# Performance work log

Hardware: AMD Instinct MI355X
Metric: run time of the kernel (lower is better)

The kernel has to match this reference:

```python
import jax, jax.numpy as jnp
import numpy as np

B, C, H, L = 8, 1, 512, 4096


def setup_inputs() -> dict:
    key = jax.random.key(0)
    k1, k2, k3, k4, k5 = jax.random.split(key, 5)
    u = jax.random.normal(k1, (B, H, L), dtype=jnp.float32)
    # SSM kernel k (C, H, L): stand-in for HippoSSKernel output, scaled so the
    # length-L convolution has O(1) variance.
    k = jax.random.normal(k2, (C, H, L), dtype=jnp.float32) * (1.0 / np.sqrt(L))
    D = jax.random.normal(k3, (C, H), dtype=jnp.float32)
    # output_linear: pointwise linear (C*H) -> H
    W = jax.random.normal(k4, (H, C * H), dtype=jnp.float32) * (1.0 / np.sqrt(C * H))
    b = jax.random.normal(k5, (H,), dtype=jnp.float32) * 0.01
    return {"u": u, "k": k, "D": D, "W": W, "b": b}


def reference(u, k, D, W, b):
    # u: (B, H, L), k: (C, H, L), D: (C, H), W: (H, C*H), b: (H,)
    Lq = u.shape[-1]
    n = 2 * Lq  # zero-padded FFT length for linear (non-circular) convolution
    k_f = jnp.fft.rfft(k, n=n)                       # (C, H, n//2+1) complex
    u_f = jnp.fft.rfft(u, n=n)                       # (B, H, n//2+1) complex
    y_f = jnp.einsum('bhl,chl->bchl', u_f, k_f)      # freq-domain multiply
    y = jnp.fft.irfft(y_f, n=n)[..., :Lq]            # (B, C, H, L)
    y = y + jnp.einsum('bhl,ch->bchl', u, D)         # skip term
    Bq, Cq, Hq, _ = y.shape
    y = y.reshape(Bq, Cq * Hq, Lq)                   # (B, C*H, L)
    y = jax.nn.gelu(y, approximate=False)            # torch GELU (erf)
    y = jnp.einsum('bcl,dc->bdl', y, W) + b[None, :, None]  # pointwise linear
    return y
```

## Files before the change

### kernel.cpp

```cpp
#include <hip/hip_runtime.h>
#include <hip/hip_bf16.h>
#include <math.h>

#define L_DIM 4096
#define H_DIM 512
#define B_DIM 8
#define SEG 2048

typedef __attribute__((ext_vector_type(8))) short short8;
typedef __attribute__((ext_vector_type(4))) float floatx4;

__device__ __forceinline__ unsigned f2bf(float f) {
    unsigned x = __float_as_uint(f);
    return (x + 0x7fffu + ((x >> 16) & 1u)) >> 16;
}

__global__ __launch_bounds__(256, 3) void conv_gelu_mfma(
    const float* __restrict__ u,
    const float* __restrict__ kk,
    const float* __restrict__ Dp,
    unsigned short* __restrict__ g)
{
    __shared__ __align__(16) unsigned short kA[4144];
    __shared__ __align__(16) unsigned short kB[4144];
    __shared__ __align__(16) unsigned short us[8][2104];

    const int h   = blockIdx.x;
    const int Lb  = blockIdx.y << 10;
    const int tid = threadIdx.x;
    const int lane = tid & 63;
    const int w   = tid >> 6;
    const int i   = lane & 15;
    const int q   = lane >> 4;
    const int b   = i & 7;
    const int s   = i >> 3;

    const float* kh = kk + (size_t)h * L_DIM;

    for (int p = tid; p < 4144; p += 256) {
        int t1 = L_DIM + 15 - p;
        int t2 = L_DIM + 14 - p;
        float v1 = (t1 >= 0 && t1 < L_DIM) ? kh[t1] : 0.0f;
        float v2 = (t2 >= 0 && t2 < L_DIM) ? kh[t2] : 0.0f;
        kA[p] = (unsigned short)f2bf(v1);
        kB[p] = (unsigned short)f2bf(v2);
    }

    floatx4 acc[8];
    #pragma unroll
    for (int t = 0; t < 8; t++) acc[t] = (floatx4){0.f, 0.f, 0.f, 0.f};

    const char* kbase = (const char*)((i & 1) ? kA : kB);
    const int aconst = 2 * (L_DIM + ((i & 1) ? 15 : 14) - i + 8 * q);
    const int basew = Lb + 32 * w;

    for (int seg = 0; seg < 2; seg++) {
        const int ms = seg * SEG;
        const int mstart = (seg == 0) ? -32 : SEG;
        const int segmax = ms + SEG - 32;
        if (seg == 1) {
            if (Lb + 992 < SEG) break;
            __syncthreads();
        }
        for (int e = tid * 4; e < 2096; e += 1024) {
            int m = ms - 32 + e;
            #pragma unroll
            for (int bb = 0; bb < 8; bb++) {
                float4 v = make_float4(0.f, 0.f, 0.f, 0.f);
                if (m >= 0 && m < L_DIM)
                    v = *(const float4*)(u + ((size_t)bb * H_DIM + h) * L_DIM + m);
                unsigned lo = f2bf(v.x) | (f2bf(v.y) << 16);
                unsigned hi = f2bf(v.z) | (f2bf(v.w) << 16);
                *(uint2*)&us[bb][e] = make_uint2(lo, hi);
            }
        }
        __syncthreads();

        const char* bbase = (const char*)&us[b][0] + 2 * (32 - ms + 16 * s + 8 * q);
        const char* ab = kbase + aconst;

        for (int c = 0; c < 4; c++) {
            const int c32 = 32 * c;
            const int rel = basew - c32;
            const int j_hi = (rel - mstart) >> 7;
            int j_lo = (rel - segmax + 127) >> 7;
            if (j_lo < -7) j_lo = -7;
            if (j_hi < j_lo) continue;
            const int n = j_hi - j_lo + 1;

            union AFrag { int x[4]; short8 v; };
            AFrag Wd[8];
            #pragma unroll
            for (int d = 1; d < 8; d++) {
                const int dd = c32 + (j_hi + d) * 128;
                if (dd >= 0) {
                    const int* ap = (const int*)(ab - 2 * dd);
                    Wd[d].x[0] = ap[0]; Wd[d].x[1] = ap[1];
                    Wd[d].x[2] = ap[2]; Wd[d].x[3] = ap[3];
                } else {
                    Wd[d].x[0] = 0; Wd[d].x[1] = 0; Wd[d].x[2] = 0; Wd[d].x[3] = 0;
                }
            }

            const char* aab = ab - 2 * c32 - 256 * j_hi;
            const char* bb0 = bbase + 2 * (rel - 128 * j_hi);

            for (int jb = 0; jb < n; jb += 8) {
                #pragma unroll
                for (int k = 0; k < 8; k++) {
                    const int jj = jb + k;
                    if (jj < n) {
                        const int dd0 = c32 + (j_hi - jj) * 128;
                        AFrag nf;
                        if (dd0 >= 0) {
                            const int* ap = (const int*)(aab + 256 * jj);
                            nf.x[0] = ap[0]; nf.x[1] = ap[1];
                            nf.x[2] = ap[2]; nf.x[3] = ap[3];
                        } else {
                            nf.x[0] = 0; nf.x[1] = 0; nf.x[2] = 0; nf.x[3] = 0;
                        }
                        Wd[(8 - k) & 7] = nf;
                        short8 bf = *(const short8*)(bb0 + 256 * jj);
                        #pragma unroll
                        for (int t = 0; t < 8; t++)
                            acc[t] = __builtin_amdgcn_mfma_f32_16x16x32_bf16(
                                Wd[(t - k) & 7].v, bf, acc[t], 0, 0, 0);
                    }
                }
            }
        }
    }

    const float Dh = Dp[h];
    #pragma unroll
    for (int t = 0; t < 8; t++) {
        const int l0 = Lb + 32 * w + 128 * t;
        const int lb2 = l0 + 16 * s + 4 * q;
        const size_t off = ((size_t)b * H_DIM + h) * L_DIM + lb2;
        float4 uv = *(const float4*)(u + off);
        float y0 = acc[t][0] + uv.x * Dh;
        float y1 = acc[t][1] + uv.y * Dh;
        float y2 = acc[t][2] + uv.z * Dh;
        float y3 = acc[t][3] + uv.w * Dh;
        const float c = 0.70710678118654752f;
        float g0 = 0.5f * y0 * (1.0f + erff(y0 * c));
        float g1 = 0.5f * y1 * (1.0f + erff(y1 * c));
        float g2 = 0.5f * y2 * (1.0f + erff(y2 * c));
        float g3 = 0.5f * y3 * (1.0f + erff(y3 * c));
        unsigned lo = f2bf(g0) | (f2bf(g1) << 16);
        unsigned hi = f2bf(g2) | (f2bf(g3) << 16);
        *(uint2*)(g + off) = make_uint2(lo, hi);
    }
}

__global__ __launch_bounds__(256, 2) void pointwise_mfma(
    const unsigned short* __restrict__ g,
    const float* __restrict__ W,
    const float* __restrict__ bias,
    float* __restrict__ out)
{
    __shared__ __align__(16) unsigned gs2[128 * 36];
    __shared__ __align__(16) unsigned short ws[256 * 72];

    const int tid = threadIdx.x;
    const int l0 = blockIdx.x * 128;
    const int d0 = blockIdx.y * 256;
    const int bz = blockIdx.z;
    const int w  = tid >> 6;
    const int lane = tid & 63;
    const int n  = lane & 15;
    const int q  = lane >> 4;

    const int p   = tid & 31;
    const int oct = tid >> 5;

    const int quarter = tid & 3;
    const int rb      = tid >> 2;

    floatx4 acc[8][4];
    #pragma unroll
    for (int mt = 0; mt < 8; mt++)
        #pragma unroll
        for (int nt = 0; nt < 4; nt++) acc[mt][nt] = (floatx4){0.f, 0.f, 0.f, 0.f};

    for (int c0 = 0; c0 < H_DIM; c0 += 64) {
        {
            const unsigned short* gp = g + ((size_t)bz * H_DIM + c0 + 2 * p) * L_DIM + l0 + 16 * oct;
            uint4 va0 = *(const uint4*)gp;
            uint4 va1 = *(const uint4*)(gp + 8);
            uint4 vb0 = *(const uint4*)(gp + L_DIM);
            uint4 vb1 = *(const uint4*)(gp + L_DIM + 8);
            #pragma unroll
            for (int half = 0; half < 2; half++) {
                const unsigned* ua = (const unsigned*)(half ? &va1 : &va0);
                const unsigned* ub = (const unsigned*)(half ? &vb1 : &vb0);
                #pragma unroll
                for (int e = 0; e < 4; e++) {
                    unsigned w0 = (ua[e] & 0xFFFFu) | (ub[e] << 16);
                    unsigned w1 = (ua[e] >> 16) | (ub[e] & 0xFFFF0000u);
                    const int lrow = 16 * oct + 8 * half + 2 * e;
                    gs2[lrow * 36 + p] = w0;
                    gs2[(lrow + 1) * 36 + p] = w1;
                }
            }
        }
        {
            #pragma unroll
            for (int gg = 0; gg < 4; gg++) {
                const int row = rb + 64 * gg;
                const float* wp = W + (size_t)(d0 + row) * H_DIM + c0 + 16 * quarter;
                float4 f0 = ((const float4*)wp)[0];
                float4 f1 = ((const float4*)wp)[1];
                float4 f2 = ((const float4*)wp)[2];
                float4 f3 = ((const float4*)wp)[3];
                unsigned o0 = f2bf(f0.x) | (f2bf(f0.y) << 16);
                unsigned o1 = f2bf(f0.z) | (f2bf(f0.w) << 16);
                unsigned o2 = f2bf(f1.x) | (f2bf(f1.y) << 16);
                unsigned o3 = f2bf(f1.z) | (f2bf(f1.w) << 16);
                unsigned o4 = f2bf(f2.x) | (f2bf(f2.y) << 16);
                unsigned o5 = f2bf(f2.z) | (f2bf(f2.w) << 16);
                unsigned o6 = f2bf(f3.x) | (f2bf(f3.y) << 16);
                unsigned o7 = f2bf(f3.z) | (f2bf(f3.w) << 16);
                *(uint4*)&ws[row * 72 + 16 * quarter]     = make_uint4(o0, o1, o2, o3);
                *(uint4*)&ws[row * 72 + 16 * quarter + 8] = make_uint4(o4, o5, o6, o7);
            }
        }
        __syncthreads();

        #pragma unroll
        for (int ks = 0; ks < 2; ks++) {
            short8 bfr[4];
            #pragma unroll
            for (int nt = 0; nt < 4; nt++)
                bfr[nt] = *(const short8*)&ws[(64 * w + 16 * nt + n) * 72 + 32 * ks + 8 * q];
            #pragma unroll
            for (int mt = 0; mt < 8; mt++) {
                union { uint4 u4; short8 v; } af;
                af.u4 = *(const uint4*)&gs2[(16 * mt + n) * 36 + 16 * ks + 4 * q];
                #pragma unroll
                for (int nt = 0; nt < 4; nt++)
                    acc[mt][nt] = __builtin_amdgcn_mfma_f32_16x16x32_bf16(af.v, bfr[nt], acc[mt][nt], 0, 0, 0);
            }
        }
        __syncthreads();
    }

    #pragma unroll
    for (int nt = 0; nt < 4; nt++) {
        const int d = d0 + 64 * w + 16 * nt + n;
        const float bb = bias[d];
        float* obase = out + ((size_t)bz * H_DIM + d) * L_DIM + l0 + 4 * q;
        #pragma unroll
        for (int mt = 0; mt < 8; mt++) {
            float4 r = make_float4(acc[mt][nt][0] + bb, acc[mt][nt][1] + bb,
                                   acc[mt][nt][2] + bb, acc[mt][nt][3] + bb);
            *(float4*)(obase + 16 * mt) = r;
        }
    }
}

extern "C" void kernel_launch(void* const* d_in, const int* in_sizes, int n_in,
                              void* d_out, int out_size, void* d_ws, size_t ws_size,
                              hipStream_t stream) {
    const float* u    = (const float*)d_in[0];
    const float* k    = (const float*)d_in[1];
    const float* D    = (const float*)d_in[2];
    const float* W    = (const float*)d_in[3];
    const float* bias = (const float*)d_in[4];
    float* out = (float*)d_out;
    unsigned short* g = (unsigned short*)d_ws;

    conv_gelu_mfma<<<dim3(H_DIM, L_DIM / 1024), 256, 0, stream>>>(u, k, D, g);
    pointwise_mfma<<<dim3(L_DIM / 128, H_DIM / 256, B_DIM), 256, 0, stream>>>(g, W, bias, out);
}
```

Baseline: 279.6 us.

## Widen conv blocks to 512 threads, pre-convert W to bf16, split pointwise warps

The conv+GELU kernel now uses 512-thread blocks that each cover 2048 output positions. The u staging is split into four 1024-wide segments to keep shared memory small, and the Toeplitz loop strides are adjusted to match. The conv kernel also converts W to bf16 once into spare workspace, so the pointwise GEMM can load bf16 weights directly instead of converting fp32 in every block. The pointwise kernel moves to 512 threads with a 2x4 warp split over the tile and wider LDS padding, which lowers per-thread accumulator pressure. The risk is lower MFMA reuse per wave and more conv blocks hitting redundant segment passes.

```diff
diff --git a/kernel.cpp b/kernel.cpp
--- a/kernel.cpp
+++ b/kernel.cpp
@@ -5,7 +5,7 @@
 #define L_DIM 4096
 #define H_DIM 512
 #define B_DIM 8
-#define SEG 2048
+#define SEG 1024
 
 typedef __attribute__((ext_vector_type(8))) short short8;
 typedef __attribute__((ext_vector_type(4))) float floatx4;
@@ -15,18 +15,20 @@
     return (x + 0x7fffu + ((x >> 16) & 1u)) >> 16;
 }
 
-__global__ __launch_bounds__(256, 3) void conv_gelu_mfma(
+__global__ __launch_bounds__(512, 8) void conv_gelu_mfma(
     const float* __restrict__ u,
     const float* __restrict__ kk,
     const float* __restrict__ Dp,
-    unsigned short* __restrict__ g)
+    unsigned short* __restrict__ g,
+    const float* __restrict__ W,
+    unsigned short* __restrict__ Wb)
 {
     __shared__ __align__(16) unsigned short kA[4144];
     __shared__ __align__(16) unsigned short kB[4144];
-    __shared__ __align__(16) unsigned short us[8][2104];
+    __shared__ __align__(16) unsigned short us[8][1080];
 
     const int h   = blockIdx.x;
-    const int Lb  = blockIdx.y << 10;
+    const int Lb  = blockIdx.y << 11;
     const int tid = threadIdx.x;
     const int lane = tid & 63;
     const int w   = tid >> 6;
@@ -35,9 +37,15 @@
     const int b   = i & 7;
     const int s   = i >> 3;
 
+    if (Wb != nullptr && blockIdx.y == 0) {
+        const float* wsrc = W + (size_t)h * H_DIM;
+        unsigned short* wdst = Wb + (size_t)h * H_DIM;
+        wdst[tid] = (unsigned short)f2bf(wsrc[tid]);
+    }
+
     const float* kh = kk + (size_t)h * L_DIM;
 
-    for (int p = tid; p < 4144; p += 256) {
+    for (int p = tid; p < 4144; p += 512) {
         int t1 = L_DIM + 15 - p;
         int t2 = L_DIM + 14 - p;
         float v1 = (t1 >= 0 && t1 < L_DIM) ? kh[t1] : 0.0f;
@@ -54,15 +62,17 @@
     const int aconst = 2 * (L_DIM + ((i & 1) ? 15 : 14) - i + 8 * q);
     const int basew = Lb + 32 * w;
 
-    for (int seg = 0; seg < 2; seg++) {
+    union AFrag { int x[4]; short8 v; };
+
+    for (int seg = 0; seg < 4; seg++) {
         const int ms = seg * SEG;
-        const int mstart = (seg == 0) ? -32 : SEG;
+        const int mstart = (seg == 0) ? -32 : ms;
         const int segmax = ms + SEG - 32;
-        if (seg == 1) {
-            if (Lb + 992 < SEG) break;
+        if (seg >= 1) {
+            if (Lb + 2016 < ms) break;
             __syncthreads();
         }
-        for (int e = tid * 4; e < 2096; e += 1024) {
+        for (int e = tid * 4; e < SEG + 48; e += 2048) {
             int m = ms - 32 + e;
             #pragma unroll
             for (int bb = 0; bb < 8; bb++) {
@@ -79,20 +89,19 @@
         const char* bbase = (const char*)&us[b][0] + 2 * (32 - ms + 16 * s + 8 * q);
         const char* ab = kbase + aconst;
 
-        for (int c = 0; c < 4; c++) {
+        for (int c = 0; c < 8; c++) {
             const int c32 = 32 * c;
             const int rel = basew - c32;
-            const int j_hi = (rel - mstart) >> 7;
-            int j_lo = (rel - segmax + 127) >> 7;
+            const int j_hi = (rel - mstart) >> 8;
+            int j_lo = (rel - segmax + 255) >> 8;
             if (j_lo < -7) j_lo = -7;
             if (j_hi < j_lo) continue;
             const int n = j_hi - j_lo + 1;
 
-            union AFrag { int x[4]; short8 v; };
             AFrag Wd[8];
             #pragma unroll
             for (int d = 1; d < 8; d++) {
-                const int dd = c32 + (j_hi + d) * 128;
+                const int dd = c32 + (j_hi + d) * 256;
                 if (dd >= 0) {
                     const int* ap = (const int*)(ab - 2 * dd);
                     Wd[d].x[0] = ap[0]; Wd[d].x[1] = ap[1];
@@ -102,25 +111,25 @@
                 }
             }
 
-            const char* aab = ab - 2 * c32 - 256 * j_hi;
-            const char* bb0 = bbase + 2 * (rel - 128 * j_hi);
+            const char* aab = ab - 2 * c32 - 512 * j_hi;
+            const char* bb0 = bbase + 2 * (rel - 256 * j_hi);
 
             for (int jb = 0; jb < n; jb += 8) {
                 #pragma unroll
                 for (int k = 0; k < 8; k++) {
                     const int jj = jb + k;
                     if (jj < n) {
-                        const int dd0 = c32 + (j_hi - jj) * 128;
+                        const int dd0 = c32 + (j_hi - jj) * 256;
                         AFrag nf;
                         if (dd0 >= 0) {
-                            const int* ap = (const int*)(aab + 256 * jj);
+                            const int* ap = (const int*)(aab + 512 * jj);
                             nf.x[0] = ap[0]; nf.x[1] = ap[1];
                             nf.x[2] = ap[2]; nf.x[3] = ap[3];
                         } else {
                             nf.x[0] = 0; nf.x[1] = 0; nf.x[2] = 0; nf.x[3] = 0;
                         }
                         Wd[(8 - k) & 7] = nf;
-                        short8 bf = *(const short8*)(bb0 + 256 * jj);
+                        short8 bf = *(const short8*)(bb0 + 512 * jj);
                         #pragma unroll
                         for (int t = 0; t < 8; t++)
                             acc[t] = __builtin_amdgcn_mfma_f32_16x16x32_bf16(
@@ -134,7 +143,7 @@
     const float Dh = Dp[h];
     #pragma unroll
     for (int t = 0; t < 8; t++) {
-        const int l0 = Lb + 32 * w + 128 * t;
+        const int l0 = Lb + 32 * w + 256 * t;
         const int lb2 = l0 + 16 * s + 4 * q;
         const size_t off = ((size_t)b * H_DIM + h) * L_DIM + lb2;
         float4 uv = *(const float4*)(u + off);
@@ -153,14 +162,16 @@
     }
 }
 
-__global__ __launch_bounds__(256, 2) void pointwise_mfma(
+template <bool PREW>
+__global__ __launch_bounds__(512, 4) void pointwise_mfma(
     const unsigned short* __restrict__ g,
+    const unsigned short* __restrict__ Wb,
     const float* __restrict__ W,
     const float* __restrict__ bias,
     float* __restrict__ out)
 {
-    __shared__ __align__(16) unsigned gs2[128 * 36];
-    __shared__ __align__(16) unsigned short ws[256 * 72];
+    __shared__ __align__(16) unsigned gs2[128 * 40];
+    __shared__ __align__(16) unsigned short ws[256 * 76];
 
     const int tid = threadIdx.x;
     const int l0 = blockIdx.x * 128;
@@ -170,44 +181,53 @@
     const int lane = tid & 63;
     const int n  = lane & 15;
     const int q  = lane >> 4;
+    const int wh = w & 1;
+    const int wd = w >> 1;
 
     const int p   = tid & 31;
-    const int oct = tid >> 5;
+    const int oct = (tid >> 5) & 7;
+    const int hi  = tid >> 8;
 
     const int quarter = tid & 3;
-    const int rb      = tid >> 2;
-
-    floatx4 acc[8][4];
+    const int rb      = (tid >> 2) & 63;
+
+    floatx4 acc[4][4];
     #pragma unroll
-    for (int mt = 0; mt < 8; mt++)
+    for (int mt = 0; mt < 4; mt++)
         #pragma unroll
         for (int nt = 0; nt < 4; nt++) acc[mt][nt] = (floatx4){0.f, 0.f, 0.f, 0.f};
 
     for (int c0 = 0; c0 < H_DIM; c0 += 64) {
         {
-            const unsigned short* gp = g + ((size_t)bz * H_DIM + c0 + 2 * p) * L_DIM + l0 + 16 * oct;
-            uint4 va0 = *(const uint4*)gp;
-            uint4 va1 = *(const uint4*)(gp + 8);
-            uint4 vb0 = *(const uint4*)(gp + L_DIM);
-            uint4 vb1 = *(const uint4*)(gp + L_DIM + 8);
-            #pragma unroll
-            for (int half = 0; half < 2; half++) {
-                const unsigned* ua = (const unsigned*)(half ? &va1 : &va0);
-                const unsigned* ub = (const unsigned*)(half ? &vb1 : &vb0);
-                #pragma unroll
-                for (int e = 0; e < 4; e++) {
-                    unsigned w0 = (ua[e] & 0xFFFFu) | (ub[e] << 16);
-                    unsigned w1 = (ua[e] >> 16) | (ub[e] & 0xFFFF0000u);
-                    const int lrow = 16 * oct + 8 * half + 2 * e;
-                    gs2[lrow * 36 + p] = w0;
-                    gs2[(lrow + 1) * 36 + p] = w1;
-                }
-            }
-        }
-        {
-            #pragma unroll
-            for (int gg = 0; gg < 4; gg++) {
-                const int row = rb + 64 * gg;
+            const unsigned short* gp = g + ((size_t)bz * H_DIM + c0 + 2 * p) * L_DIM
+                                         + l0 + 16 * oct + 8 * hi;
+            uint4 va = *(const uint4*)gp;
+            uint4 vb = *(const uint4*)(gp + L_DIM);
+            const unsigned* ua = (const unsigned*)&va;
+            const unsigned* ub = (const unsigned*)&vb;
+            #pragma unroll
+            for (int e = 0; e < 4; e++) {
+                unsigned w0 = (ua[e] & 0xFFFFu) | (ub[e] << 16);
+                unsigned w1 = (ua[e] >> 16) | (ub[e] & 0xFFFF0000u);
+                const int lrow = 16 * oct + 8 * hi + 2 * e;
+                gs2[lrow * 40 + p] = w0;
+                gs2[(lrow + 1) * 40 + p] = w1;
+            }
+        }
+        if (PREW) {
+            #pragma unroll
+            for (int g2 = 0; g2 < 2; g2++) {
+                const int row = rb + 64 * (2 * hi + g2);
+                const unsigned short* wp = Wb + (size_t)(d0 + row) * H_DIM + c0 + 16 * quarter;
+                uint4 w0 = ((const uint4*)wp)[0];
+                uint4 w1 = ((const uint4*)wp)[1];
+                *(uint4*)&ws[row * 76 + 16 * quarter]     = w0;
+                *(uint4*)&ws[row * 76 + 16 * quarter + 8] = w1;
+            }
+        } else {
+            #pragma unroll
+            for (int g2 = 0; g2 < 2; g2++) {
+                const int row = rb + 64 * (2 * hi + g2);
                 const float* wp = W + (size_t)(d0 + row) * H_DIM + c0 + 16 * quarter;
                 float4 f0 = ((const float4*)wp)[0];
                 float4 f1 = ((const float4*)wp)[1];
@@ -221,8 +241,8 @@
                 unsigned o5 = f2bf(f2.z) | (f2bf(f2.w) << 16);
                 unsigned o6 = f2bf(f3.x) | (f2bf(f3.y) << 16);
                 unsigned o7 = f2bf(f3.z) | (f2bf(f3.w) << 16);
-                *(uint4*)&ws[row * 72 + 16 * quarter]     = make_uint4(o0, o1, o2, o3);
-                *(uint4*)&ws[row * 72 + 16 * quarter + 8] = make_uint4(o4, o5, o6, o7);
+                *(uint4*)&ws[row * 76 + 16 * quarter]     = make_uint4(o0, o1, o2, o3);
+                *(uint4*)&ws[row * 76 + 16 * quarter + 8] = make_uint4(o4, o5, o6, o7);
             }
         }
         __syncthreads();
@@ -232,11 +252,11 @@
             short8 bfr[4];
             #pragma unroll
             for (int nt = 0; nt < 4; nt++)
-                bfr[nt] = *(const short8*)&ws[(64 * w + 16 * nt + n) * 72 + 32 * ks + 8 * q];
-            #pragma unroll
-            for (int mt = 0; mt < 8; mt++) {
+                bfr[nt] = *(const short8*)&ws[(64 * wd + 16 * nt + n) * 76 + 32 * ks + 8 * q];
+            #pragma unroll
+            for (int mt = 0; mt < 4; mt++) {
                 union { uint4 u4; short8 v; } af;
-                af.u4 = *(const uint4*)&gs2[(16 * mt + n) * 36 + 16 * ks + 4 * q];
+                af.u4 = *(const uint4*)&gs2[(64 * wh + 16 * mt + n) * 40 + 16 * ks + 4 * q];
                 #pragma unroll
                 for (int nt = 0; nt < 4; nt++)
                     acc[mt][nt] = __builtin_amdgcn_mfma_f32_16x16x32_bf16(af.v, bfr[nt], acc[mt][nt], 0, 0, 0);
@@ -247,11 +267,11 @@
 
     #pragma unroll
     for (int nt = 0; nt < 4; nt++) {
-        const int d = d0 + 64 * w + 16 * nt + n;
+        const int d = d0 + 64 * wd + 16 * nt + n;
         const float bb = bias[d];
-        float* obase = out + ((size_t)bz * H_DIM + d) * L_DIM + l0 + 4 * q;
+        float* obase = out + ((size_t)bz * H_DIM + d) * L_DIM + l0 + 64 * wh + 4 * q;
         #pragma unroll
-        for (int mt = 0; mt < 8; mt++) {
+        for (int mt = 0; mt < 4; mt++) {
             float4 r = make_float4(acc[mt][nt][0] + bb, acc[mt][nt][1] + bb,
                                    acc[mt][nt][2] + bb, acc[mt][nt][3] + bb);
             *(float4*)(obase + 16 * mt) = r;
@@ -270,6 +290,14 @@
     float* out = (float*)d_out;
     unsigned short* g = (unsigned short*)d_ws;
 
-    conv_gelu_mfma<<<dim3(H_DIM, L_DIM / 1024), 256, 0, stream>>>(u, k, D, g);
-    pointwise_mfma<<<dim3(L_DIM / 128, H_DIM / 256, B_DIM), 256, 0, stream>>>(g, W, bias, out);
+    const size_t g_bytes = (size_t)B_DIM * H_DIM * L_DIM * sizeof(unsigned short);
+    const size_t w_bytes = (size_t)H_DIM * H_DIM * sizeof(unsigned short);
+    const bool prew = ws_size >= g_bytes + w_bytes;
+    unsigned short* Wb = prew ? (unsigned short*)((char*)d_ws + g_bytes) : nullptr;
+
+    conv_gelu_mfma<<<dim3(H_DIM, L_DIM / 2048), 512, 0, stream>>>(u, k, D, g, W, Wb);
+    if (prew)
+        pointwise_mfma<true><<<dim3(L_DIM / 128, H_DIM / 256, B_DIM), 512, 0, stream>>>(g, Wb, W, bias, out);
+    else
+        pointwise_mfma<false><<<dim3(L_DIM / 128, H_DIM / 256, B_DIM), 512, 0, stream>>>(g, nullptr, W, bias, out);
 }
```

After: 791.1 us. 183% more time.
